# Kernel tuning notes

Hardware: AMD Instinct MI355X
Metric: run time of the kernel (lower is better)

Reference implementation:

```python
import jax, jax.numpy as jnp
import numpy as np

K = 9  # kernel size == stride, asserted by the module


def setup_inputs() -> dict:
    key = jax.random.key(0)
    k1, k2, k3 = jax.random.split(key, 3)
    x = jax.random.normal(k1, (4, 16, 8192), dtype=jnp.float32)
    W = jax.random.normal(k2, (16, 16, K), dtype=jnp.float32) * 0.1  # conv1d weight [out,in,K]
    b = jax.random.normal(k3, (16,), dtype=jnp.float32) * 0.1       # conv1d bias [out]
    return {"x": x, "W": W, "b": b}


def reference(x, W, b):
    # x: [B, C, N]; sampling_type='all', similarity='Col', aggregation='Col',
    # magnitude='euclidean', no shuffle, no padding, no coordinate encoding.
    B, C, N = x.shape
    # squared euclidean distance matrix [B, N, N]
    ns = jnp.sum(x * x, axis=1)                      # [B, N]
    dot = jnp.einsum('bcn,bcm->bnm', x, x)           # [B, N, N]
    dist = jnp.maximum(ns[:, :, None] + ns[:, None, :] - 2.0 * dot, 0.0)
    # diagonal filled with -0.1 so each token is its own nearest neighbor
    eye = jnp.eye(N, dtype=bool)
    dist = jnp.where(eye[None, :, :], jnp.float32(-0.1), dist)
    # euclidean -> maximum=False -> take K smallest distances
    _, idx = jax.lax.top_k(-dist, K)                 # idx: [B, N, K]
    # gather neighbor features: prime[b, :, n, k] = x[b, :, idx[b, n, k]]
    neigh = jax.vmap(lambda xb, ib: xb[:, ib])(x, idx)   # [B, C, N, K]
    # Conv1d(kernel=K, stride=K, padding=0) over the flattened [B, C, N*K] prime
    # tensor == per-token contraction over (C, K)
    out = jnp.einsum('bcnk,ock->bon', neigh, W) + b[None, :, None]  # [B, out, N]
    return out
```

## Files before the change

### kernel.cpp

```cpp
#include <hip/hip_runtime.h>
#include <hip/hip_bf16.h>
#include <math.h>

#define NB 4
#define NC 16
#define NN 8192
#define NK 9
#define CANDN 128
#define MR (NN / 4)
#define HPAD 129

typedef short s16x8 __attribute__((ext_vector_type(8)));
typedef float f32x4 __attribute__((ext_vector_type(4)));

#define OFF_XS   2097152u
#define OFF_NS   4194304u
#define OFF_NK   4325376u
#define OFF_NBR  4456448u
#define OFF_FLAG 5046272u
#define OFF_CAND 5177344u

__global__ void prep_kernel(const float* __restrict__ x,
                            float* __restrict__ xt,
                            float* __restrict__ ns32,
                            float* __restrict__ nk,
                            unsigned short* __restrict__ xs) {
    int t = blockIdx.x * 256 + threadIdx.x;
    int b = t >> 13, m = t & (NN - 1);
    const float* xb = x + (size_t)b * NC * NN;
    float v[NC];
#pragma unroll
    for (int c = 0; c < NC; ++c) v[c] = xb[(size_t)c * NN + m];
    float s = __fmul_rn(v[0], v[0]);
#pragma unroll
    for (int c = 1; c < NC; ++c) s = __fadd_rn(s, __fmul_rn(v[c], v[c]));
    float* o = xt + (size_t)t * NC;
#pragma unroll
    for (int c = 0; c < NC; ++c) o[c] = v[c];
    ns32[t] = s;
    nk[t] = 128.0f + 0.5f * s;
    unsigned short* xo = xs + (size_t)t * 32;
#pragma unroll
    for (int c = 0; c < NC; ++c) {
        __hip_bfloat16 h = __float2bfloat16(v[c]);
        float hf = __bfloat162float(h);
        __hip_bfloat16 l = __float2bfloat16(v[c] - hf);
        xo[c] = *(unsigned short*)&h;
        xo[16 + c] = *(unsigned short*)&l;
    }
}

__device__ __forceinline__ s16x8 negbf(s16x8 v) {
    s16x8 r;
#pragma unroll
    for (int i = 0; i < 8; ++i) r[i] = (short)(v[i] ^ (short)0x8000);
    return r;
}

__global__ __launch_bounds__(256, 8) void topk_kernel(
        const unsigned short* __restrict__ xs, const float* __restrict__ nk,
        unsigned short* __restrict__ cand, unsigned* __restrict__ flags) {
    __shared__ __align__(16) unsigned hist[16 * HPAD];
    __shared__ __align__(16) unsigned short list[16][CANDN];
    __shared__ unsigned cnt[16];
    __shared__ unsigned Bbin[16];
    const int tid = threadIdx.x;
    const int L = tid & 63;
    const int wq = tid >> 6;
    const int b = blockIdx.x >> 9;
    const int n0 = (blockIdx.x & 511) * 16;
    const int lrow = L & 15;
    const int lk = L >> 4;

    {
        for (int i = tid; i < 16 * HPAD; i += 256) hist[i] = 0u;
        unsigned* lp = (unsigned*)&list[0][0];
        for (int i = tid; i < 16 * CANDN / 2; i += 256) lp[i] = 0xFFFFFFFFu;
        if (tid < 16) { cnt[tid] = 0u; Bbin[tid] = 127u; }
    }
    __syncthreads();

    const char* xsb = (const char*)xs + (size_t)b * NN * 64;
    const float* nkb = nk + (size_t)b * NN;
    const char* nkc = (const char*)nkb;

    const int khalf = (lk & 1) * 16;
    const int r0 = n0 + lrow;
    const s16x8 bhi0 = negbf(*(const s16x8*)(xsb + (size_t)r0 * 64 + khalf));
    const s16x8 blo0 = negbf(*(const s16x8*)(xsb + (size_t)r0 * 64 + 32 + khalf));

    const float base8_0 = 8.0f * (256.0f - nkb[r0]);

    const int m0 = wq * MR;
    const int voffA0 = (m0 + lrow) * 64 + lk * 16;
    const int voffK0 = (m0 + lk * 4) * 4;

    {
        int vA = voffA0, vK = voffK0;
        for (int t = 0; t < 64; ++t) {
            const s16x8 a = *(const s16x8*)(xsb + vA);
            const f32x4 nkv = *(const f32x4*)(nkc + vK);
            f32x4 acc0 = __builtin_amdgcn_mfma_f32_16x16x32_bf16(a, bhi0, nkv, 0, 0, 0);
            acc0 = __builtin_amdgcn_mfma_f32_16x16x32_bf16(a, blo0, acc0, 0, 0, 0);
#pragma unroll
            for (int r = 0; r < 4; ++r) {
                const float rr = fmaf(acc0[r], 8.0f, -base8_0);
                if (rr < 127.0f) {
                    const unsigned bin = (unsigned)fmaxf(rr, 0.0f);
                    atomicAdd(&hist[lrow * HPAD + bin], 1u);
                }
            }
            vA += 1024;
            vK += 64;
        }
    }
    __syncthreads();
    if (tid < 16) {
        unsigned cum = 0;
        unsigned Bv = 127u;
        for (int j = 0; j < 127; ++j) {
            cum += hist[tid * HPAD + j];
            if (cum >= 12u) { Bv = (unsigned)j; break; }
        }
        Bbin[tid] = Bv;
    }
    __syncthreads();
    const unsigned B0 = Bbin[lrow];
    const float thrf0 = (base8_0 + (float)B0 + 1.25f) * 0.125f;

    {
        int vA = voffA0, vK = voffK0;
        for (int t = 0; t < MR / 16; ++t) {
            const s16x8 a = *(const s16x8*)(xsb + vA);
            const f32x4 nkv = *(const f32x4*)(nkc + vK);
            f32x4 acc0 = __builtin_amdgcn_mfma_f32_16x16x32_bf16(a, bhi0, nkv, 0, 0, 0);
            acc0 = __builtin_amdgcn_mfma_f32_16x16x32_bf16(a, blo0, acc0, 0, 0, 0);
            const float mn0 = fminf(fminf(acc0[0], acc0[1]),
                                    fminf(acc0[2], acc0[3]));
            if (mn0 < thrf0) {
#pragma unroll
                for (int r = 0; r < 4; ++r) {
                    if (acc0[r] < thrf0) {
                        const unsigned m =
                            (unsigned)(m0 + t * 16 + lk * 4 + r);
                        const unsigned idx = atomicAdd(&cnt[lrow], 1u);
                        if (idx < CANDN)
                            list[lrow][idx] = (unsigned short)m;
                    }
                }
            }
            vA += 1024;
            vK += 64;
        }
    }
    __syncthreads();

    {
        const int rr = tid >> 4, seg = tid & 15;
        const unsigned grow = (unsigned)(b * NN + n0 + rr);
        const uint4* src =
            (const uint4*)((const char*)&list[0][0] + rr * 256 + seg * 16);
        uint4* dst = (uint4*)((char*)cand + (size_t)grow * 256 + seg * 16);
        dst[0] = src[0];
    }
    if (tid < 16) {
        const bool bad = (cnt[tid] > (unsigned)CANDN) || (Bbin[tid] == 127u);
        flags[b * NN + n0 + tid] = bad ? 0xFFFFFFFFu : cnt[tid];
    }
}

__global__ __launch_bounds__(256) void rerank_kernel(
        const float* __restrict__ xt, const float* __restrict__ ns32,
        const unsigned short* __restrict__ cand,
        const unsigned* __restrict__ flags,
        unsigned short* __restrict__ nbr) {
    __shared__ unsigned long long mk[64][36];
    const int tid = threadIdx.x;
    const int lr = tid >> 2;
    const int j = tid & 3;
    const int row = blockIdx.x * 64 + lr;
    const int b = row >> 13;
    const int n = row & (NN - 1);
    const float* xb = xt + (size_t)b * NN * NC;
    const float* xrow = xb + (size_t)n * NC;
    float xv[NC];
#pragma unroll
    for (int c = 0; c < NC; ++c) xv[c] = xrow[c];
    const float nsn = ns32[row];
    const float* nsb = ns32 + b * NN;

    unsigned long long lst[NK];
#pragma unroll
    for (int i = 0; i < NK; ++i) lst[i] = ~0ULL;

    auto consider = [&](int m) {
        const float* col = xb + (size_t)m * NC;
        float dot = 0.0f;
#pragma unroll
        for (int c = 0; c < NC; ++c)
            dot = fmaf(xv[c], col[c], dot);
        float dist = __fsub_rn(__fadd_rn(nsn, nsb[m]), __fmul_rn(2.0f, dot));
        dist = fmaxf(dist, 0.0f);
        const unsigned k32 = (m == n) ? 0u
                                      : (__float_as_uint(dist) | 0x80000000u);
        unsigned long long key = ((unsigned long long)k32 << 32) | (unsigned)m;
        if (key < lst[NK - 1]) {
#pragma unroll
            for (int i = 0; i < NK; ++i) {
                unsigned long long aa = lst[i];
                bool sm = key < aa;
                unsigned long long lo = sm ? key : aa;
                unsigned long long hi = sm ? aa : key;
                lst[i] = lo;
                key = hi;
            }
        }
    };

    const unsigned nv = flags[row];
    if (nv == 0xFFFFFFFFu) {
        for (int m = j * (NN / 4); m < (j + 1) * (NN / 4); ++m) consider(m);
    } else {
        const unsigned short* cl = cand + (size_t)row * CANDN;
        for (unsigned jj = (unsigned)j; jj < nv; jj += 4) consider(cl[jj]);
    }
#pragma unroll
    for (int i = 0; i < NK; ++i) mk[lr][j * NK + i] = lst[i];
    __syncthreads();
    if (j == 0) {
        unsigned long long fin[NK];
#pragma unroll
        for (int i = 0; i < NK; ++i) fin[i] = ~0ULL;
        for (int s = 0; s < 4 * NK; ++s) {
            unsigned long long key = mk[lr][s];
            if (key < fin[NK - 1]) {
#pragma unroll
                for (int i = 0; i < NK; ++i) {
                    unsigned long long aa = fin[i];
                    bool sm = key < aa;
                    unsigned long long lo = sm ? key : aa;
                    unsigned long long hi = sm ? aa : key;
                    fin[i] = lo;
                    key = hi;
                }
            }
        }
        unsigned short* o = nbr + (size_t)row * NK;
#pragma unroll
        for (int k = 0; k < NK; ++k) o[k] = (unsigned short)(fin[k] & 0xFFFFu);
    }
}

__global__ __launch_bounds__(256) void conv_kernel(
        const float* __restrict__ xt, const unsigned short* __restrict__ nbr,
        const float* __restrict__ W, const float* __restrict__ bias,
        float* __restrict__ out) {
    const int tid = threadIdx.x;
    const int ob = blockIdx.x >> 7;
    const int rb = blockIdx.x & 127;
    const int row = rb * 256 + tid;
    const int b = rb >> 5;
    const int n = row & (NN - 1);
    const float* xb = xt + (size_t)b * NN * NC;
    const float* Wo = W + ob * (NC * NK);
    const unsigned short* nl = nbr + (size_t)row * NK;

    float acc = bias[ob];
    for (int k = 0; k < NK; ++k) {
        const float* col = xb + (size_t)nl[k] * NC;
        float cv[NC];
#pragma unroll
        for (int c = 0; c < NC; ++c) cv[c] = col[c];
#pragma unroll
        for (int c = 0; c < NC; ++c)
            acc = fmaf(Wo[c * NK + k], cv[c], acc);
    }
    out[(size_t)b * NC * NN + (size_t)ob * NN + n] = acc;
}

extern "C" void kernel_launch(void* const* d_in, const int* in_sizes, int n_in,
                              void* d_out, int out_size, void* d_ws, size_t ws_size,
                              hipStream_t stream) {
    const float* x = (const float*)d_in[0];
    const float* W = (const float*)d_in[1];
    const float* bias = (const float*)d_in[2];
    float* out = (float*)d_out;

    char* ws = (char*)d_ws;
    float* xt = (float*)ws;
    unsigned short* xs = (unsigned short*)(ws + OFF_XS);
    float* ns32 = (float*)(ws + OFF_NS);
    float* nk = (float*)(ws + OFF_NK);
    unsigned short* nbr = (unsigned short*)(ws + OFF_NBR);
    unsigned* flags = (unsigned*)(ws + OFF_FLAG);
    unsigned short* cand = (unsigned short*)(ws + OFF_CAND);

    prep_kernel<<<128, 256, 0, stream>>>(x, xt, ns32, nk, xs);
    topk_kernel<<<2048, 256, 0, stream>>>(xs, nk, cand, flags);
    rerank_kernel<<<512, 256, 0, stream>>>(xt, ns32, cand, flags, nbr);
    conv_kernel<<<2048, 256, 0, stream>>>(xt, nbr, W, bias, out);
}
```

Baseline: 210.9 us.

## Process 64 query rows per topk block to reuse candidate tile loads

The top-k filtering kernel now handles 64 query rows per block instead of 16. Each loaded candidate A-fragment and norm vector feeds four MFMA tiles, so global and L2 reads of the candidate matrix drop by four. The grid shrinks from 2048 to 512 blocks and occupancy is lowered to 2 blocks per CU. Shared memory grows fourfold for the histograms and lists, and register pressure rises, which cuts parallelism: 512 blocks on 256 CUs gives only about 2 blocks per CU.

```diff
diff --git a/kernel.cpp b/kernel.cpp
--- a/kernel.cpp
+++ b/kernel.cpp
@@ -9,6 +9,7 @@
 #define CANDN 128
 #define MR (NN / 4)
 #define HPAD 129
+#define NROW 64
 
 typedef short s16x8 __attribute__((ext_vector_type(8)));
 typedef float f32x4 __attribute__((ext_vector_type(4)));
@@ -57,26 +58,26 @@
     return r;
 }
 
-__global__ __launch_bounds__(256, 8) void topk_kernel(
+__global__ __launch_bounds__(256, 2) void topk_kernel(
         const unsigned short* __restrict__ xs, const float* __restrict__ nk,
         unsigned short* __restrict__ cand, unsigned* __restrict__ flags) {
-    __shared__ __align__(16) unsigned hist[16 * HPAD];
-    __shared__ __align__(16) unsigned short list[16][CANDN];
-    __shared__ unsigned cnt[16];
-    __shared__ unsigned Bbin[16];
+    __shared__ __align__(16) unsigned hist[NROW * HPAD];
+    __shared__ __align__(16) unsigned short list[NROW][CANDN];
+    __shared__ unsigned cnt[NROW];
+    __shared__ unsigned Bbin[NROW];
     const int tid = threadIdx.x;
     const int L = tid & 63;
     const int wq = tid >> 6;
-    const int b = blockIdx.x >> 9;
-    const int n0 = (blockIdx.x & 511) * 16;
+    const int b = blockIdx.x >> 7;
+    const int n0 = (blockIdx.x & 127) * NROW;
     const int lrow = L & 15;
     const int lk = L >> 4;
 
     {
-        for (int i = tid; i < 16 * HPAD; i += 256) hist[i] = 0u;
+        for (int i = tid; i < NROW * HPAD; i += 256) hist[i] = 0u;
         unsigned* lp = (unsigned*)&list[0][0];
-        for (int i = tid; i < 16 * CANDN / 2; i += 256) lp[i] = 0xFFFFFFFFu;
-        if (tid < 16) { cnt[tid] = 0u; Bbin[tid] = 127u; }
+        for (int i = tid; i < NROW * CANDN / 2; i += 256) lp[i] = 0xFFFFFFFFu;
+        if (tid < NROW) { cnt[tid] = 0u; Bbin[tid] = 127u; }
     }
     __syncthreads();
 
@@ -85,11 +86,15 @@
     const char* nkc = (const char*)nkb;
 
     const int khalf = (lk & 1) * 16;
-    const int r0 = n0 + lrow;
-    const s16x8 bhi0 = negbf(*(const s16x8*)(xsb + (size_t)r0 * 64 + khalf));
-    const s16x8 blo0 = negbf(*(const s16x8*)(xsb + (size_t)r0 * 64 + 32 + khalf));
-
-    const float base8_0 = 8.0f * (256.0f - nkb[r0]);
+    s16x8 bhi[4], blo[4];
+    float base8[4];
+#pragma unroll
+    for (int nt = 0; nt < 4; ++nt) {
+        const int rr = n0 + nt * 16 + lrow;
+        bhi[nt] = negbf(*(const s16x8*)(xsb + (size_t)rr * 64 + khalf));
+        blo[nt] = negbf(*(const s16x8*)(xsb + (size_t)rr * 64 + 32 + khalf));
+        base8[nt] = 8.0f * (256.0f - nkb[rr]);
+    }
 
     const int m0 = wq * MR;
     const int voffA0 = (m0 + lrow) * 64 + lk * 16;
@@ -100,14 +105,18 @@
         for (int t = 0; t < 64; ++t) {
             const s16x8 a = *(const s16x8*)(xsb + vA);
             const f32x4 nkv = *(const f32x4*)(nkc + vK);
-            f32x4 acc0 = __builtin_amdgcn_mfma_f32_16x16x32_bf16(a, bhi0, nkv, 0, 0, 0);
-            acc0 = __builtin_amdgcn_mfma_f32_16x16x32_bf16(a, blo0, acc0, 0, 0, 0);
-#pragma unroll
-            for (int r = 0; r < 4; ++r) {
-                const float rr = fmaf(acc0[r], 8.0f, -base8_0);
-                if (rr < 127.0f) {
-                    const unsigned bin = (unsigned)fmaxf(rr, 0.0f);
-                    atomicAdd(&hist[lrow * HPAD + bin], 1u);
+#pragma unroll
+            for (int nt = 0; nt < 4; ++nt) {
+                f32x4 acc = __builtin_amdgcn_mfma_f32_16x16x32_bf16(a, bhi[nt], nkv, 0, 0, 0);
+                acc = __builtin_amdgcn_mfma_f32_16x16x32_bf16(a, blo[nt], acc, 0, 0, 0);
+                const int hrow = nt * 16 + lrow;
+#pragma unroll
+                for (int r = 0; r < 4; ++r) {
+                    const float rr = fmaf(acc[r], 8.0f, -base8[nt]);
+                    if (rr < 127.0f) {
+                        const unsigned bin = (unsigned)fmaxf(rr, 0.0f);
+                        atomicAdd(&hist[hrow * HPAD + bin], 1u);
+                    }
                 }
             }
             vA += 1024;
@@ -115,7 +124,7 @@
         }
     }
     __syncthreads();
-    if (tid < 16) {
+    if (tid < NROW) {
         unsigned cum = 0;
         unsigned Bv = 127u;
         for (int j = 0; j < 127; ++j) {
@@ -125,27 +134,33 @@
         Bbin[tid] = Bv;
     }
     __syncthreads();
-    const unsigned B0 = Bbin[lrow];
-    const float thrf0 = (base8_0 + (float)B0 + 1.25f) * 0.125f;
+    float thrf[4];
+#pragma unroll
+    for (int nt = 0; nt < 4; ++nt)
+        thrf[nt] = (base8[nt] + (float)Bbin[nt * 16 + lrow] + 1.25f) * 0.125f;
 
     {
         int vA = voffA0, vK = voffK0;
         for (int t = 0; t < MR / 16; ++t) {
             const s16x8 a = *(const s16x8*)(xsb + vA);
             const f32x4 nkv = *(const f32x4*)(nkc + vK);
-            f32x4 acc0 = __builtin_amdgcn_mfma_f32_16x16x32_bf16(a, bhi0, nkv, 0, 0, 0);
-            acc0 = __builtin_amdgcn_mfma_f32_16x16x32_bf16(a, blo0, acc0, 0, 0, 0);
-            const float mn0 = fminf(fminf(acc0[0], acc0[1]),
-                                    fminf(acc0[2], acc0[3]));
-            if (mn0 < thrf0) {
-#pragma unroll
-                for (int r = 0; r < 4; ++r) {
-                    if (acc0[r] < thrf0) {
-                        const unsigned m =
-                            (unsigned)(m0 + t * 16 + lk * 4 + r);
-                        const unsigned idx = atomicAdd(&cnt[lrow], 1u);
-                        if (idx < CANDN)
-                            list[lrow][idx] = (unsigned short)m;
+#pragma unroll
+            for (int nt = 0; nt < 4; ++nt) {
+                f32x4 acc = __builtin_amdgcn_mfma_f32_16x16x32_bf16(a, bhi[nt], nkv, 0, 0, 0);
+                acc = __builtin_amdgcn_mfma_f32_16x16x32_bf16(a, blo[nt], acc, 0, 0, 0);
+                const float mn = fminf(fminf(acc[0], acc[1]),
+                                       fminf(acc[2], acc[3]));
+                if (mn < thrf[nt]) {
+                    const int hrow = nt * 16 + lrow;
+#pragma unroll
+                    for (int r = 0; r < 4; ++r) {
+                        if (acc[r] < thrf[nt]) {
+                            const unsigned m =
+                                (unsigned)(m0 + t * 16 + lk * 4 + r);
+                            const unsigned idx = atomicAdd(&cnt[hrow], 1u);
+                            if (idx < CANDN)
+                                list[hrow][idx] = (unsigned short)m;
+                        }
                     }
                 }
             }
@@ -155,15 +170,17 @@
     }
     __syncthreads();
 
-    {
-        const int rr = tid >> 4, seg = tid & 15;
+#pragma unroll
+    for (int p = 0; p < 4; ++p) {
+        const int rr = (tid >> 4) + p * 16;
+        const int seg = tid & 15;
         const unsigned grow = (unsigned)(b * NN + n0 + rr);
         const uint4* src =
             (const uint4*)((const char*)&list[0][0] + rr * 256 + seg * 16);
         uint4* dst = (uint4*)((char*)cand + (size_t)grow * 256 + seg * 16);
         dst[0] = src[0];
     }
-    if (tid < 16) {
+    if (tid < NROW) {
         const bool bad = (cnt[tid] > (unsigned)CANDN) || (Bbin[tid] == 127u);
         flags[b * NN + n0 + tid] = bad ? 0xFFFFFFFFu : cnt[tid];
     }
@@ -296,7 +313,7 @@
     unsigned short* cand = (unsigned short*)(ws + OFF_CAND);
 
     prep_kernel<<<128, 256, 0, stream>>>(x, xt, ns32, nk, xs);
-    topk_kernel<<<2048, 256, 0, stream>>>(xs, nk, cand, flags);
+    topk_kernel<<<512, 256, 0, stream>>>(xs, nk, cand, flags);
     rerank_kernel<<<512, 256, 0, stream>>>(xt, ns32, cand, flags, nbr);
     conv_kernel<<<2048, 256, 0, stream>>>(xt, nbr, W, bias, out);
 }
```

After: 232.7 us. +10.3%, slower.
